# Kernel optimization log

Hardware: AMD Instinct MI355X
Metric: run time of the kernel (lower is better)

## Reference

```python
import jax, jax.numpy as jnp
import numpy as np

B, S, D = 2, 2048, 1024
H, DK, DV = 16, 64, 64


def setup_inputs() -> dict:
    key = jax.random.key(0)
    ks = jax.random.split(key, 12)
    s = 0.02
    return {
        "query": jax.random.normal(ks[0], (B, S, D), jnp.float32),
        "key": jax.random.normal(ks[1], (B, S, D), jnp.float32),
        "value": jax.random.normal(ks[2], (B, S, D), jnp.float32),
        "mask": jax.random.randint(ks[3], (B, S, S), 0, 2, jnp.int32),
        "Wq": jax.random.normal(ks[4], (D, H * DK), jnp.float32) * s,
        "bq": jnp.zeros((H * DK,), jnp.float32),
        "Wk": jax.random.normal(ks[5], (D, H * DK), jnp.float32) * s,
        "bk": jnp.zeros((H * DK,), jnp.float32),
        "Wv": jax.random.normal(ks[6], (D, H * DV), jnp.float32) * s,
        "bv": jnp.zeros((H * DV,), jnp.float32),
        "Wo": jax.random.normal(ks[7], (H * DV, D), jnp.float32) * s,
        "bo": jnp.zeros((D,), jnp.float32),
    }


def reference(query, key, value, mask, Wq, bq, Wk, bk, Wv, bv, Wo, bo):
    temperature = jnp.sqrt(jnp.asarray(DK, query.dtype))
    # projections: [B,S,H*dk] -> [B,H,S,dk]
    q = (query @ Wq + bq).reshape(B, S, H, DK).transpose(0, 2, 1, 3)
    k = (key @ Wk + bk).reshape(B, S, H, DK).transpose(0, 2, 1, 3)
    v = (value @ Wv + bv).reshape(B, S, H, DV).transpose(0, 2, 1, 3)
    # energy: [B,H,Sq,Skv]
    energy = jnp.einsum("bhqd,bhkd->bhqk", q, k) / temperature
    energy = jnp.where(mask[:, None, :, :] == 0, jnp.asarray(-10000.0, energy.dtype), energy)
    attention = jax.nn.softmax(energy, axis=-1)
    attention = jnp.where(jnp.isnan(attention), jnp.asarray(0.0, attention.dtype), attention)
    out = jnp.einsum("bhqk,bhkd->bhqd", attention, v)  # dropout p=0 (eval)
    out = out.transpose(0, 2, 1, 3).reshape(B, S, H * DV)
    out = out @ Wo + bo
    return (out, attention)
```

## Files before the change

kernel.cpp:

```cpp
#include <hip/hip_runtime.h>
#include <stdint.h>


typedef __attribute__((ext_vector_type(8))) __bf16 bf16x8;
typedef __attribute__((ext_vector_type(8))) short short8;
typedef __attribute__((ext_vector_type(4))) float f32x4;

static __device__ __forceinline__ f32x4 mfma_bf16(short8 a, short8 b, f32x4 c) {
  return __builtin_amdgcn_mfma_f32_16x16x32_bf16(
      __builtin_bit_cast(bf16x8, a), __builtin_bit_cast(bf16x8, b), c, 0, 0, 0);
}

static __device__ __forceinline__ unsigned short f2bf(float f) {
  unsigned int u = __float_as_uint(f);
  u += 0x7fffu + ((u >> 16) & 1u);
  return (unsigned short)(u >> 16);
}

static __device__ __forceinline__ void gload_lds16(const void* g, void* l) {
  __builtin_amdgcn_global_load_lds(
      (__attribute__((address_space(1))) void*)(uintptr_t)(g),
      (__attribute__((address_space(3))) void*)(uintptr_t)(l), 16, 0, 0);
}

__global__ __launch_bounds__(256) void conv_f32_bf16(
    const float* q, const float* k, const float* v,
    unsigned short* oq, unsigned short* ok, unsigned short* ov) {
  const float* src = (blockIdx.z == 0) ? q : (blockIdx.z == 1) ? k : v;
  unsigned short* dst = (blockIdx.z == 0) ? oq : (blockIdx.z == 1) ? ok : ov;
  const int i = (blockIdx.x * 256 + threadIdx.x) * 8;
  const float4 a = *(const float4*)&src[i];
  const float4 b = *(const float4*)&src[i + 4];
  unsigned short r[8] = {f2bf(a.x), f2bf(a.y), f2bf(a.z), f2bf(a.w),
                         f2bf(b.x), f2bf(b.y), f2bf(b.z), f2bf(b.w)};
  *(uint4*)&dst[i] = *(uint4*)r;
}

__global__ __launch_bounds__(256) void transpose_w(
    const float* w0, const float* w1, const float* w2, const float* w3,
    unsigned short* o0, unsigned short* o1,
    unsigned short* o2, unsigned short* o3) {
  const float* src = (blockIdx.z == 0) ? w0 : (blockIdx.z == 1) ? w1
                                         : (blockIdx.z == 2) ? w2 : w3;
  unsigned short* dst = (blockIdx.z == 0) ? o0 : (blockIdx.z == 1) ? o1
                                           : (blockIdx.z == 2) ? o2 : o3;
  __shared__ unsigned short tile[64 * 66];
  const int t = threadIdx.x;
  const int r0 = blockIdx.y * 64, c0 = blockIdx.x * 64;
#pragma unroll
  for (int i = 0; i < 4; ++i) {
    const int slot = i * 256 + t;
    const int row = slot >> 4, cg = slot & 15;
    const float4 v = *(const float4*)&src[(r0 + row) * 1024 + c0 + cg * 4];
    unsigned int p0 = (unsigned int)f2bf(v.x) | ((unsigned int)f2bf(v.y) << 16);
    unsigned int p1 = (unsigned int)f2bf(v.z) | ((unsigned int)f2bf(v.w) << 16);
    unsigned int* dp = (unsigned int*)&tile[row * 66 + cg * 4];
    dp[0] = p0;
    dp[1] = p1;
  }
  __syncthreads();
#pragma unroll
  for (int i = 0; i < 2; ++i) {
    const int slot = i * 256 + t;
    const int orow = slot >> 3, kg = slot & 7;
    unsigned short vals[8];
#pragma unroll
    for (int j = 0; j < 8; ++j) vals[j] = tile[(kg * 8 + j) * 66 + orow];
    *(uint4*)&dst[(c0 + orow) * 1024 + r0 + kg * 8] = *(uint4*)vals;
  }
}

__global__ __launch_bounds__(256) void mask_prep(const int* __restrict__ mask,
                                                 unsigned long long* __restrict__ bits) {
  const int wid = (blockIdx.x * 256 + threadIdx.x) >> 6;
  const int lane = threadIdx.x & 63;
  for (int w = wid; w < 131072; w += 2048) {
    const int m = mask[w * 64 + lane];
    const unsigned long long b = __ballot(m != 0);
    if (lane == 0) bits[w] = b;
  }
}

struct GArg {
  const unsigned short* A;
  const unsigned short* BT;
  const float* bias;
  void* C;
  int mode;
};

__global__ __launch_bounds__(256) void gemm_bt(GArg ga, GArg gb, GArg gc) {
  const GArg g = (blockIdx.z == 0) ? ga : (blockIdx.z == 1) ? gb : gc;
  __shared__ alignas(16) unsigned short ash[128 * 64];
  __shared__ alignas(16) unsigned short bsh[128 * 64];
  const int t = threadIdx.x;
  const int wave = t >> 6, lane = t & 63;
  const int m0 = blockIdx.y * 128, n0 = blockIdx.x * 128;
  const int wm = (wave >> 1) * 64, wn = (wave & 1) * 64;
  const int c = lane & 15, gq = lane >> 4;
  const int srow = wave * 8 + (lane >> 3);
  const int scol = (lane & 7) * 8;

  f32x4 zero = {0.f, 0.f, 0.f, 0.f};
  f32x4 acc[4][4];
#pragma unroll
  for (int i = 0; i < 4; ++i)
#pragma unroll
    for (int j = 0; j < 4; ++j) acc[i][j] = zero;

  for (int kk = 0; kk < 16; ++kk) {
    __syncthreads();
    const int kbase = kk * 64;
#pragma unroll
    for (int i = 0; i < 4; ++i) {
      gload_lds16(&g.A[(m0 + i * 32 + srow) * 1024 + kbase + scol],
                  &ash[(i * 32 + wave * 8) * 64]);
      gload_lds16(&g.BT[(n0 + i * 32 + srow) * 1024 + kbase + scol],
                  &bsh[(i * 32 + wave * 8) * 64]);
    }
    __syncthreads();
#pragma unroll
    for (int ks = 0; ks < 2; ++ks) {
      short8 af[4], bf[4];
#pragma unroll
      for (int mt = 0; mt < 4; ++mt)
        af[mt] = *(const short8*)&ash[(wm + mt * 16 + c) * 64 + ks * 32 + gq * 8];
#pragma unroll
      for (int nt = 0; nt < 4; ++nt)
        bf[nt] = *(const short8*)&bsh[(wn + nt * 16 + c) * 64 + ks * 32 + gq * 8];
#pragma unroll
      for (int mt = 0; mt < 4; ++mt)
#pragma unroll
        for (int nt = 0; nt < 4; ++nt)
          acc[mt][nt] = mfma_bf16(af[mt], bf[nt], acc[mt][nt]);
    }
  }
#pragma unroll
  for (int nt = 0; nt < 4; ++nt) {
    const int gcol = n0 + wn + nt * 16 + c;
    const float bia = g.bias[gcol];
#pragma unroll
    for (int mt = 0; mt < 4; ++mt) {
#pragma unroll
      for (int r = 0; r < 4; ++r) {
        const int grow = m0 + wm + mt * 16 + gq * 4 + r;
        const float v = acc[mt][nt][r] + bia;
        if (g.mode == 0) {
          ((unsigned short*)g.C)[grow * 1024 + gcol] = f2bf(v);
        } else if (g.mode == 1) {
          ((unsigned short*)g.C)[((grow >> 11) << 21) + (gcol << 11) + (grow & 2047)] =
              f2bf(v);
        } else {
          ((float*)g.C)[grow * 1024 + gcol] = v;
        }
      }
    }
  }
}

__global__ __launch_bounds__(256) void attn_kern(
    const unsigned short* __restrict__ Qb, const unsigned short* __restrict__ Kb,
    const unsigned short* __restrict__ Vt, const unsigned long long* __restrict__ mbits,
    float* __restrict__ att, unsigned short* __restrict__ Obuf) {
  const int id0 = blockIdx.x + 32 * (blockIdx.y + 16 * blockIdx.z);
  const int id = (id0 & 7) * 128 + (id0 >> 3);
  const int qt = id & 31, h = (id >> 5) & 15, b = id >> 9;
  const int t = threadIdx.x, wave = t >> 6, lane = t & 63;
  const int q0 = qt * 64;
  const int c = lane & 15, gq = lane >> 4;
  const int srow = lane >> 3;
  const int scol_sw = ((lane & 7) ^ srow) * 8;
  const float SCALE = 0.125f * 1.44269504088896341f;

  __shared__ alignas(16) unsigned short kt[2][64 * 64];
  __shared__ alignas(16) unsigned short vt[2][64 * 64];
  __shared__ alignas(16) float psf[4 * 16 * 64];

  auto stage_k = [&](int kvt, int bu) {
#pragma unroll
    for (int i = 0; i < 2; ++i)
      gload_lds16(&Kb[(b * 2048 + kvt * 64 + wave * 16 + i * 8 + srow) * 1024 +
                      h * 64 + scol_sw],
                  &kt[bu][(wave * 16 + i * 8) * 64]);
  };
  auto stage_v = [&](int kvt, int bu) {
#pragma unroll
    for (int i = 0; i < 2; ++i)
      gload_lds16(&Vt[(b << 21) + (h * 64 + wave * 16 + i * 8 + srow) * 2048 +
                      kvt * 64 + scol_sw],
                  &vt[bu][(wave * 16 + i * 8) * 64]);
  };
  auto rdcol = [&](int ks) { return (((ks * 4 + gq) ^ (c & 7)) * 8); };

  stage_k(0, 0);

  unsigned long long* msk = (unsigned long long*)psf;
  {
    const int row = t >> 2, c8 = (t & 3) * 8;
    const unsigned long long* src = &mbits[(unsigned)(b * 2048 + q0 + row) * 32 + c8];
#pragma unroll
    for (int j = 0; j < 8; ++j) msk[row * 32 + c8 + j] = src[j];
  }
  unsigned long long mlo[4], mhi[4];
#pragma unroll
  for (int r = 0; r < 4; ++r) {
    const int row = wave * 16 + gq * 4 + r;
    unsigned long long lo = 0, hi = 0;
#pragma unroll
    for (int kvi = 0; kvi < 16; ++kvi) {
      const unsigned long long w0 = msk[row * 32 + kvi] >> c;
      const unsigned long long w1 = msk[row * 32 + 16 + kvi] >> c;
      const unsigned long long n0 =
          (w0 & 1) | ((w0 >> 15) & 2) | ((w0 >> 30) & 4) | ((w0 >> 45) & 8);
      const unsigned long long n1 =
          (w1 & 1) | ((w1 >> 15) & 2) | ((w1 >> 30) & 4) | ((w1 >> 45) & 8);
      lo |= n0 << (kvi * 4);
      hi |= n1 << (kvi * 4);
    }
    mlo[r] = lo;
    mhi[r] = hi;
  }

  short8 aq[2];
  {
    const unsigned short* qrow = &Qb[(b * 2048 + q0 + wave * 16 + c) * 1024 + h * 64];
    aq[0] = *(const short8*)&qrow[gq * 8];
    aq[1] = *(const short8*)&qrow[32 + gq * 8];
  }

  asm volatile("s_waitcnt vmcnt(0) lgkmcnt(0)" ::: "memory");
  __builtin_amdgcn_s_barrier();
  __builtin_amdgcn_sched_barrier(0);

  const f32x4 zero = {0.f, 0.f, 0.f, 0.f};
  float lsum[4] = {0.f, 0.f, 0.f, 0.f};
  int buf = 0;

#pragma unroll 1
  for (int kv = 0; kv < 32; ++kv) {
    if (kv < 31) {
      stage_k(kv + 1, buf ^ 1);
      asm volatile("s_waitcnt vmcnt(2)" ::: "memory");
    } else {
      asm volatile("s_waitcnt vmcnt(0)" ::: "memory");
    }
    __builtin_amdgcn_s_barrier();
    __builtin_amdgcn_sched_barrier(0);

    f32x4 s[4];
#pragma unroll
    for (int nt = 0; nt < 4; ++nt) s[nt] = zero;
    __builtin_amdgcn_s_setprio(1);
#pragma unroll
    for (int ks = 0; ks < 2; ++ks)
#pragma unroll
      for (int nt = 0; nt < 4; ++nt) {
        const short8 bk = *(const short8*)&kt[buf][(nt * 16 + c) * 64 + rdcol(ks)];
        s[nt] = mfma_bf16(aq[ks], bk, s[nt]);
      }
    __builtin_amdgcn_s_setprio(0);
#pragma unroll
    for (int r = 0; r < 4; ++r) {
      const unsigned long long mr = (kv < 16) ? mlo[r] : mhi[r];
      const unsigned nib = (unsigned)(mr >> ((kv & 15) * 4)) & 0xFu;
#pragma unroll
      for (int nt = 0; nt < 4; ++nt) {
        const float e = ((nib >> nt) & 1u) ? s[nt][r] * SCALE : -30.f;
        lsum[r] += __builtin_amdgcn_exp2f(e);
      }
    }
    asm volatile("s_waitcnt lgkmcnt(0)" ::: "memory");
    __builtin_amdgcn_s_barrier();
    __builtin_amdgcn_sched_barrier(0);
    buf ^= 1;
  }

  float linv[4];
#pragma unroll
  for (int r = 0; r < 4; ++r) {
    float v = lsum[r];
    v += __shfl_xor(v, 1);
    v += __shfl_xor(v, 2);
    v += __shfl_xor(v, 4);
    v += __shfl_xor(v, 8);
    linv[r] = 1.0f / v;
  }

  f32x4 o[4];
#pragma unroll
  for (int nt = 0; nt < 4; ++nt) o[nt] = zero;

  stage_k(0, buf);
  stage_v(0, buf);
  asm volatile("s_waitcnt vmcnt(0)" ::: "memory");
  __builtin_amdgcn_s_barrier();
  __builtin_amdgcn_sched_barrier(0);

#pragma unroll 1
  for (int kv = 0; kv < 32; ++kv) {
    if (kv < 31) {
      stage_k(kv + 1, buf ^ 1);
      stage_v(kv + 1, buf ^ 1);
      asm volatile("s_waitcnt vmcnt(4)" ::: "memory");
    } else {
      asm volatile("s_waitcnt vmcnt(4)" ::: "memory");
    }
    __builtin_amdgcn_s_barrier();
    __builtin_amdgcn_sched_barrier(0);

    f32x4 s[4];
#pragma unroll
    for (int nt = 0; nt < 4; ++nt) s[nt] = zero;
    __builtin_amdgcn_s_setprio(1);
#pragma unroll
    for (int ks = 0; ks < 2; ++ks)
#pragma unroll
      for (int nt = 0; nt < 4; ++nt) {
        const short8 bk = *(const short8*)&kt[buf][(nt * 16 + c) * 64 + rdcol(ks)];
        s[nt] = mfma_bf16(aq[ks], bk, s[nt]);
      }
    __builtin_amdgcn_s_setprio(0);
#pragma unroll
    for (int r = 0; r < 4; ++r) {
      const unsigned long long mr = (kv < 16) ? mlo[r] : mhi[r];
      const unsigned nib = (unsigned)(mr >> ((kv & 15) * 4)) & 0xFu;
#pragma unroll
      for (int nt = 0; nt < 4; ++nt) {
        const float e = ((nib >> nt) & 1u) ? s[nt][r] * SCALE : -30.f;
        const float p = __builtin_amdgcn_exp2f(e) * linv[r];
        psf[wave * 1024 + (gq * 4 + r) * 64 + nt * 16 + c] = p;
      }
    }
#pragma unroll
    for (int ks = 0; ks < 2; ++ks) {
      const float4 f0 = *(const float4*)&psf[wave * 1024 + c * 64 + ks * 32 + gq * 8];
      const float4 f1 = *(const float4*)&psf[wave * 1024 + c * 64 + ks * 32 + gq * 8 + 4];
      unsigned short pr[8] = {f2bf(f0.x), f2bf(f0.y), f2bf(f0.z), f2bf(f0.w),
                              f2bf(f1.x), f2bf(f1.y), f2bf(f1.z), f2bf(f1.w)};
      const short8 ap = *(const short8*)pr;
      __builtin_amdgcn_s_setprio(1);
#pragma unroll
      for (int nt = 0; nt < 4; ++nt) {
        const short8 bv = *(const short8*)&vt[buf][(nt * 16 + c) * 64 + rdcol(ks)];
        o[nt] = mfma_bf16(ap, bv, o[nt]);
      }
      __builtin_amdgcn_s_setprio(0);
    }
#pragma unroll
    for (int pass = 0; pass < 4; ++pass) {
      const int row = pass * 4 + (lane >> 4);
      const int col4 = lane & 15;
      const float4 pv = *(const float4*)&psf[wave * 1024 + row * 64 + col4 * 4];
      *(float4*)&att[((long)((b * 16 + h) * 2048 + q0 + wave * 16 + row)) * 2048 +
                     kv * 64 + col4 * 4] = pv;
    }
    asm volatile("s_waitcnt lgkmcnt(0)" ::: "memory");
    __builtin_amdgcn_s_barrier();
    __builtin_amdgcn_sched_barrier(0);
    buf ^= 1;
  }

#pragma unroll
  for (int nt = 0; nt < 4; ++nt)
#pragma unroll
    for (int r = 0; r < 4; ++r) {
      const int row = q0 + wave * 16 + gq * 4 + r;
      Obuf[(b * 2048 + row) * 1024 + h * 64 + nt * 16 + c] = f2bf(o[nt][r]);
    }
}

extern "C" void kernel_launch(void* const* d_in, const int* in_sizes, int n_in,
                              void* d_out, int out_size, void* d_ws, size_t ws_size,
                              hipStream_t stream) {
  const float* query = (const float*)d_in[0];
  const float* key   = (const float*)d_in[1];
  const float* value = (const float*)d_in[2];
  const int* mask    = (const int*)d_in[3];
  const float* Wq = (const float*)d_in[4];
  const float* bq = (const float*)d_in[5];
  const float* Wk = (const float*)d_in[6];
  const float* bk = (const float*)d_in[7];
  const float* Wv = (const float*)d_in[8];
  const float* bv = (const float*)d_in[9];
  const float* Wo = (const float*)d_in[10];
  const float* bo = (const float*)d_in[11];

  float* out = (float*)d_out;
  float* att = out + 4194304;

  char* ws = (char*)d_ws;
  const size_t MB = 1u << 20;
  unsigned short* Aq   = (unsigned short*)(ws);
  unsigned short* Ak   = (unsigned short*)(ws + 8 * MB);
  unsigned short* Av   = (unsigned short*)(ws + 16 * MB);
  unsigned short* Qb   = (unsigned short*)(ws + 24 * MB);
  unsigned short* Kb   = (unsigned short*)(ws + 32 * MB);
  unsigned short* Vt   = (unsigned short*)(ws + 40 * MB);
  unsigned short* Obuf = (unsigned short*)(ws + 48 * MB);
  unsigned short* WqT  = (unsigned short*)(ws + 56 * MB);
  unsigned short* WkT  = (unsigned short*)(ws + 58 * MB);
  unsigned short* WvT  = (unsigned short*)(ws + 60 * MB);
  unsigned short* WoT  = (unsigned short*)(ws + 62 * MB);
  unsigned long long* mbits = (unsigned long long*)(ws + 64 * MB);

  conv_f32_bf16<<<dim3(2048, 1, 3), 256, 0, stream>>>(query, key, value, Aq, Ak, Av);
  transpose_w<<<dim3(16, 16, 4), 256, 0, stream>>>(Wq, Wk, Wv, Wo, WqT, WkT, WvT, WoT);
  mask_prep<<<dim3(512), 256, 0, stream>>>(mask, mbits);

  GArg gq{Aq, WqT, bq, Qb, 0};
  GArg gk{Ak, WkT, bk, Kb, 0};
  GArg gv{Av, WvT, bv, Vt, 1};
  gemm_bt<<<dim3(8, 32, 3), 256, 0, stream>>>(gq, gk, gv);

  attn_kern<<<dim3(32, 16, 2), 256, 0, stream>>>(Qb, Kb, Vt, mbits, att, Obuf);

  GArg go{Obuf, WoT, bo, out, 2};
  gemm_bt<<<dim3(8, 32, 1), 256, 0, stream>>>(go, go, go);
}
```

Measured before the change: 837.2 us.

## Store attention probabilities directly from registers and stage P as swizzled bf16

The second pass of the attention kernel now writes each probability straight from registers to the global attention output, instead of staging fp32 values in LDS and writing float4 rows. P is stored in LDS as bf16 with an XOR swizzle, which shrinks shared memory. The mask scratch reuses the V buffer, launch bounds request four blocks per SM, and the vmcnt waits are raised to cover the extra outstanding stores. Scalar 4-byte global stores are less coalesced than float4 rows, which may hurt the 512MB attention write, and the waitcnt counts must match the number of stores in flight.

Result: no change. 832.8 us (-0.5%).

```diff
diff --git a/kernel.cpp b/kernel.cpp
--- a/kernel.cpp
+++ b/kernel.cpp
@@ -158,7 +158,7 @@
   }
 }
 
-__global__ __launch_bounds__(256) void attn_kern(
+__global__ __launch_bounds__(256, 4) void attn_kern(
     const unsigned short* __restrict__ Qb, const unsigned short* __restrict__ Kb,
     const unsigned short* __restrict__ Vt, const unsigned long long* __restrict__ mbits,
     float* __restrict__ att, unsigned short* __restrict__ Obuf) {
@@ -174,7 +174,7 @@
 
   __shared__ alignas(16) unsigned short kt[2][64 * 64];
   __shared__ alignas(16) unsigned short vt[2][64 * 64];
-  __shared__ alignas(16) float psf[4 * 16 * 64];
+  __shared__ alignas(16) unsigned short psfb[4][16 * 64];
 
   auto stage_k = [&](int kvt, int bu) {
 #pragma unroll
@@ -194,13 +194,14 @@
 
   stage_k(0, 0);
 
-  unsigned long long* msk = (unsigned long long*)psf;
+  unsigned long long* msk = (unsigned long long*)vt;
   {
     const int row = t >> 2, c8 = (t & 3) * 8;
     const unsigned long long* src = &mbits[(unsigned)(b * 2048 + q0 + row) * 32 + c8];
 #pragma unroll
     for (int j = 0; j < 8; ++j) msk[row * 32 + c8 + j] = src[j];
   }
+  __builtin_amdgcn_sched_barrier(0);
   unsigned long long mlo[4], mhi[4];
 #pragma unroll
   for (int r = 0; r < 4; ++r) {
@@ -296,14 +297,21 @@
   __builtin_amdgcn_s_barrier();
   __builtin_amdgcn_sched_barrier(0);
 
+  float* attb[4];
+#pragma unroll
+  for (int r = 0; r < 4; ++r)
+    attb[r] = att + (long)((b * 16 + h) * 2048 + q0 + wave * 16 + gq * 4 + r) * 2048 + c;
+
+  unsigned short* pw = &psfb[wave][0];
+
 #pragma unroll 1
   for (int kv = 0; kv < 32; ++kv) {
     if (kv < 31) {
       stage_k(kv + 1, buf ^ 1);
       stage_v(kv + 1, buf ^ 1);
-      asm volatile("s_waitcnt vmcnt(4)" ::: "memory");
+      asm volatile("s_waitcnt vmcnt(20)" ::: "memory");
     } else {
-      asm volatile("s_waitcnt vmcnt(4)" ::: "memory");
+      asm volatile("s_waitcnt vmcnt(16)" ::: "memory");
     }
     __builtin_amdgcn_s_barrier();
     __builtin_amdgcn_sched_barrier(0);
@@ -320,24 +328,28 @@
         s[nt] = mfma_bf16(aq[ks], bk, s[nt]);
       }
     __builtin_amdgcn_s_setprio(0);
+
 #pragma unroll
     for (int r = 0; r < 4; ++r) {
       const unsigned long long mr = (kv < 16) ? mlo[r] : mhi[r];
       const unsigned nib = (unsigned)(mr >> ((kv & 15) * 4)) & 0xFu;
+      const int prow = gq * 4 + r;
+      const int sw = (prow & 7) << 3;
 #pragma unroll
       for (int nt = 0; nt < 4; ++nt) {
         const float e = ((nib >> nt) & 1u) ? s[nt][r] * SCALE : -30.f;
         const float p = __builtin_amdgcn_exp2f(e) * linv[r];
-        psf[wave * 1024 + (gq * 4 + r) * 64 + nt * 16 + c] = p;
-      }
-    }
+        attb[r][nt * 16] = p;
+        pw[prow * 64 + ((nt * 16 + c) ^ sw)] = f2bf(p);
+      }
+      attb[r] += 64;
+    }
+    __builtin_amdgcn_sched_barrier(0);
+
 #pragma unroll
     for (int ks = 0; ks < 2; ++ks) {
-      const float4 f0 = *(const float4*)&psf[wave * 1024 + c * 64 + ks * 32 + gq * 8];
-      const float4 f1 = *(const float4*)&psf[wave * 1024 + c * 64 + ks * 32 + gq * 8 + 4];
-      unsigned short pr[8] = {f2bf(f0.x), f2bf(f0.y), f2bf(f0.z), f2bf(f0.w),
-                              f2bf(f1.x), f2bf(f1.y), f2bf(f1.z), f2bf(f1.w)};
-      const short8 ap = *(const short8*)pr;
+      const short8 ap =
+          *(const short8*)&pw[c * 64 + ((ks * 32 + gq * 8) ^ ((c & 7) << 3))];
       __builtin_amdgcn_s_setprio(1);
 #pragma unroll
       for (int nt = 0; nt < 4; ++nt) {
@@ -345,14 +357,6 @@
         o[nt] = mfma_bf16(ap, bv, o[nt]);
       }
       __builtin_amdgcn_s_setprio(0);
-    }
-#pragma unroll
-    for (int pass = 0; pass < 4; ++pass) {
-      const int row = pass * 4 + (lane >> 4);
-      const int col4 = lane & 15;
-      const float4 pv = *(const float4*)&psf[wave * 1024 + row * 64 + col4 * 4];
-      *(float4*)&att[((long)((b * 16 + h) * 2048 + q0 + wave * 16 + row)) * 2048 +
-                     kv * 64 + col4 * 4] = pv;
     }
     asm volatile("s_waitcnt lgkmcnt(0)" ::: "memory");
     __builtin_amdgcn_s_barrier();
```
